# Optimization experiments

Measured on AMD Instinct MI355X. Metric: run time of the kernel, lower is better.

Reference implementation:

```python
import jax, jax.numpy as jnp
import numpy as np

N = 8192
F_IN = 690
F_OUT = 690
H = 3
ALPHA = 0.2  # LeakyReLU negative slope
NEG_INF = -9e15


def setup_inputs() -> dict:
    key = jax.random.key(0)
    k1, k2, k3, k4 = jax.random.split(key, 4)
    x = jax.random.normal(k1, (N, F_IN), dtype=jnp.float32)
    adj = jax.random.randint(k2, (N, N), 0, 2, dtype=jnp.int32)
    adj = adj.at[jnp.arange(N), jnp.arange(N)].set(1)  # self-loops, as in eye() init
    # Xavier-ish scaled params, stacked over heads
    W = jax.random.normal(k3, (H, F_IN, F_OUT), dtype=jnp.float32) * 0.05
    a = jax.random.normal(k4, (H, 2 * F_OUT, 1), dtype=jnp.float32) * 0.05
    return {"x": x, "adj": adj, "W": W, "a": a}


def reference(x, adj, W, a):
    # Wh per head: [H, N, F_OUT]
    Wh = jnp.einsum('nf,hfo->hno', x, W)
    # Additive decomposition of concat-based score: e_ij = leakyrelu(a1_i + a2_j)
    a1 = jnp.einsum('hno,ho->hn', Wh, a[:, :F_OUT, 0])  # [H, N]
    a2 = jnp.einsum('hno,ho->hn', Wh, a[:, F_OUT:, 0])  # [H, N]
    e = jax.nn.leaky_relu(a1[:, :, None] + a2[:, None, :], negative_slope=ALPHA)  # [H, N, N]
    e = jnp.where(adj[None, :, :] > 0, e, NEG_INF)
    attn = jax.nn.softmax(e, axis=-1)
    h_prime = jnp.einsum('hnm,hmo->hno', attn, Wh)  # [H, N, F_OUT]
    # GAT(concat=False): mean over heads, then ELU (dropout is identity in eval)
    y = jax.nn.elu(jnp.mean(h_prime, axis=0))  # [N, F_OUT]
    return y
```

## Files before the change

kernel.cpp:

```cpp
#include <hip/hip_runtime.h>
#include <hip/hip_bf16.h>
#include <stdint.h>

#define NN 8192
#define FD 690
#define NH 3
#define KPAD 704
#define OPAD 768
#define USTRIDE 704
#define KS 2
#define LOG2E 1.4426950408889634f

typedef __attribute__((ext_vector_type(8))) short bf16x8;
typedef __attribute__((ext_vector_type(4))) float f32x4;

typedef __attribute__((address_space(1))) const void gas_t;
typedef __attribute__((address_space(3))) void las_t;

__device__ __forceinline__ void async_ld16(const void* g, void* l) {
  __builtin_amdgcn_global_load_lds((gas_t*)g, (las_t*)l, 16, 0, 0);
}

__device__ __forceinline__ float bf2f(unsigned short u) {
  return __uint_as_float(((unsigned int)u) << 16);
}
__device__ __forceinline__ unsigned short f2bf(float f) {
  __hip_bfloat16 h = __float2bfloat16(f);
  return *reinterpret_cast<unsigned short*>(&h);
}
__device__ __forceinline__ float selbit(float e, uint32_t lo, uint32_t hi) {
  uint64_t m = ((uint64_t)hi << 32) | lo;
  float r;
  asm("v_cndmask_b32 %0, 0, %1, %2" : "=v"(r) : "v"(e), "s"(m));
  return r;
}

__global__ __launch_bounds__(256) void k_cast(const float* __restrict__ x,
                                              const float* __restrict__ W,
                                              unsigned short* __restrict__ xb,
                                              unsigned short* __restrict__ wt) {
  int idx = blockIdx.x * 256 + threadIdx.x;
  if (idx < NN * KPAD) {
    int n = idx / KPAD, f = idx - n * KPAD;
    float v = (f < FD) ? x[(size_t)n * FD + f] : 0.f;
    xb[idx] = f2bf(v);
    return;
  }
  idx -= NN * KPAD;
  if (idx >= NH * OPAD * KPAD) return;
  int h = idx / (OPAD * KPAD);
  int rem = idx - h * OPAD * KPAD;
  int o = rem / KPAD, f = rem - o * KPAD;
  float v = (o < FD && f < FD) ? W[((size_t)h * FD + f) * FD + o] : 0.f;
  wt[idx] = f2bf(v);
}

__global__ __launch_bounds__(256) void k_pack(const int* __restrict__ adj,
                                              uint64_t* __restrict__ bm) {
  int wid = (blockIdx.x * 256 + threadIdx.x) >> 6;
  int lane = threadIdx.x & 63;
  int i = wid >> 7, wj = wid & 127;
  int v = adj[(int64_t)i * NN + wj * 64 + lane];
  uint64_t m = __ballot(v > 0);
  if (lane == 0) bm[i * 128 + wj] = m;
}

__global__ __launch_bounds__(512) void k_gemm_wht(const unsigned short* __restrict__ wt,
                                                  const unsigned short* __restrict__ xb,
                                                  const float* __restrict__ a,
                                                  unsigned short* __restrict__ wht,
                                                  float* __restrict__ a1acc,
                                                  float* __restrict__ a2acc) {
  const int m0 = blockIdx.x * 128;
  const int n0 = blockIdx.y * 256;
  const int h  = blockIdx.z;
  const int tid = threadIdx.x;
  const int w = tid >> 6, l = tid & 63;
  const int wm = w >> 2, wn = w & 3;
  __shared__ unsigned short As[128 * 64];
  __shared__ unsigned short Bs[256 * 64];
  const unsigned short* Ag = wt + (size_t)h * OPAD * KPAD;
  f32x4 acc[4][4] = {};
  for (int kt = 0; kt < KPAD / 64; ++kt) {
    const int k0 = kt * 64;
#pragma unroll
    for (int r = 0; r < 2; ++r) {
      const unsigned short* g = Ag + (size_t)(m0 + r * 64 + w * 8 + (l >> 3)) * KPAD + k0 + (l & 7) * 8;
      async_ld16(g, &As[(r * 64 + w * 8) * 64]);
    }
#pragma unroll
    for (int r = 0; r < 4; ++r) {
      const unsigned short* g = xb + (size_t)(n0 + r * 64 + w * 8 + (l >> 3)) * KPAD + k0 + (l & 7) * 8;
      async_ld16(g, &Bs[(r * 64 + w * 8) * 64]);
    }
    __syncthreads();
#pragma unroll
    for (int ks = 0; ks < 2; ++ks) {
      bf16x8 af[4], bfr[4];
#pragma unroll
      for (int mi = 0; mi < 4; ++mi)
        af[mi] = *reinterpret_cast<const bf16x8*>(
            &As[(wm * 64 + mi * 16 + (l & 15)) * 64 + ks * 32 + (l >> 4) * 8]);
#pragma unroll
      for (int ni = 0; ni < 4; ++ni)
        bfr[ni] = *reinterpret_cast<const bf16x8*>(
            &Bs[(wn * 64 + ni * 16 + (l & 15)) * 64 + ks * 32 + (l >> 4) * 8]);
#pragma unroll
      for (int mi = 0; mi < 4; ++mi)
#pragma unroll
        for (int ni = 0; ni < 4; ++ni)
          acc[mi][ni] = __builtin_amdgcn_mfma_f32_16x16x32_bf16(af[mi], bfr[ni], acc[mi][ni], 0, 0, 0);
    }
    __syncthreads();
  }
  unsigned short* Wh = wht + (size_t)h * OPAD * NN;
#pragma unroll
  for (int mi = 0; mi < 4; ++mi)
#pragma unroll
    for (int j = 0; j < 4; ++j) {
      int o = m0 + wm * 64 + mi * 16 + (l >> 4) * 4 + j;
#pragma unroll
      for (int ni = 0; ni < 4; ++ni) {
        int n = n0 + wn * 64 + ni * 16 + (l & 15);
        float val = (o == FD) ? 1.0f : acc[mi][ni][j];
        Wh[(size_t)o * NN + n] = f2bf(val);
      }
    }
  const float* ap1 = a + h * 2 * FD;
  const float* ap2 = ap1 + FD;
  float av1[4][4], av2[4][4];
#pragma unroll
  for (int mi = 0; mi < 4; ++mi)
#pragma unroll
    for (int j = 0; j < 4; ++j) {
      int o = m0 + wm * 64 + mi * 16 + (l >> 4) * 4 + j;
      bool ok = (o < FD);
      av1[mi][j] = ok ? ap1[o] : 0.f;
      av2[mi][j] = ok ? ap2[o] : 0.f;
    }
#pragma unroll
  for (int ni = 0; ni < 4; ++ni) {
    float p1 = 0.f, p2 = 0.f;
#pragma unroll
    for (int mi = 0; mi < 4; ++mi)
#pragma unroll
      for (int j = 0; j < 4; ++j) {
        p1 += acc[mi][ni][j] * av1[mi][j];
        p2 += acc[mi][ni][j] * av2[mi][j];
      }
    int n = n0 + wn * 64 + ni * 16 + (l & 15);
    unsafeAtomicAdd(&a1acc[h * NN + n], p1);
    unsafeAtomicAdd(&a2acc[h * NN + n], p2);
  }
}

__global__ __launch_bounds__(256) void k_exp(const float* __restrict__ a1acc,
                                             const float* __restrict__ a2acc,
                                             float* __restrict__ e1s, float* __restrict__ f1s,
                                             float* __restrict__ e2s, float* __restrict__ f2s) {
  int i = blockIdx.x * 256 + threadIdx.x;
  if (i >= NH * NN) return;
  float s1 = a1acc[i] * LOG2E, s2 = a2acc[i] * LOG2E;
  e1s[i] = exp2f(s1);
  f1s[i] = exp2f(0.2f * s1);
  e2s[i] = exp2f(s2);
  f2s[i] = exp2f(0.2f * s2);
}

__global__ __launch_bounds__(512, 4) void k_pv(const unsigned short* __restrict__ wht,
                                               const float* __restrict__ e1s,
                                               const float* __restrict__ f1s,
                                               const float* __restrict__ e2s,
                                               const float* __restrict__ f2s,
                                               const uint64_t* __restrict__ bm,
                                               float* __restrict__ U) {
  const int m0 = blockIdx.x * 64;
  const int n0 = blockIdx.y * 384;
  const int h    = blockIdx.z / KS;
  const int kseg = blockIdx.z % KS;
  const int tid = threadIdx.x;
  const int w = tid >> 6, l = tid & 63;
  const int wu = __builtin_amdgcn_readfirstlane(w);
  __shared__ unsigned short As[64 * 64];
  __shared__ unsigned short Bs[384 * 64];
  const unsigned short* Bg = wht + (size_t)h * OPAD * NN;
  const uint64_t* bmw = bm + (size_t)(m0 + wu * 8) * 128;
  float E1v[8], F1v[8];
#pragma unroll
  for (int r = 0; r < 8; ++r) {
    E1v[r] = e1s[h * NN + m0 + wu * 8 + r];
    F1v[r] = f1s[h * NN + m0 + wu * 8 + r];
  }

  const int kt0 = kseg * (NN / 64 / KS);
  const int ktend = kt0 + NN / 64 / KS;

  f32x4 acc[4][3] = {};

  for (int kt = kt0; kt < ktend; ++kt) {
    const int k0 = kt * 64;
    const float e2v = e2s[h * NN + k0 + l];
    const float f2v = f2s[h * NN + k0 + l];
#pragma unroll
    for (int call = 0; call < 6; ++call) {
      int c = call * 512 + tid;
      int row = c >> 3;
      int kb  = c & 7;
      int kbs = kb ^ (row & 7);
      const unsigned short* g = Bg + (size_t)(n0 + row) * NN + k0 + kbs * 8;
      async_ld16(g, &Bs[(size_t)c * 8]);
    }
#pragma unroll
    for (int r = 0; r < 8; ++r) {
      uint64_t mrow = bmw[(size_t)r * 128 + kt];
      uint32_t mlo = __builtin_amdgcn_readfirstlane((uint32_t)mrow);
      uint32_t mhi = __builtin_amdgcn_readfirstlane((uint32_t)(mrow >> 32));
      float e = fmaxf(E1v[r] * e2v, F1v[r] * f2v);
      e = selbit(e, mlo, mhi);
      As[(wu * 8 + r) * 64 + (l ^ (r << 3))] = f2bf(e);
    }
    __syncthreads();

#pragma unroll
    for (int ks = 0; ks < 2; ++ks) {
      bf16x8 af[4], bfr[3];
#pragma unroll
      for (int mi = 0; mi < 4; ++mi) {
        int row = mi * 16 + (l & 15);
        af[mi] = *reinterpret_cast<const bf16x8*>(
            &As[row * 64 + (((ks * 4 + (l >> 4)) ^ (row & 7)) * 8)]);
      }
#pragma unroll
      for (int ni = 0; ni < 3; ++ni) {
        int row = w * 48 + ni * 16 + (l & 15);
        bfr[ni] = *reinterpret_cast<const bf16x8*>(
            &Bs[row * 64 + (((ks * 4 + (l >> 4)) ^ (row & 7)) * 8)]);
      }
#pragma unroll
      for (int mi = 0; mi < 4; ++mi)
#pragma unroll
        for (int ni = 0; ni < 3; ++ni)
          acc[mi][ni] = __builtin_amdgcn_mfma_f32_16x16x32_bf16(af[mi], bfr[ni], acc[mi][ni], 0, 0, 0);
    }
    __syncthreads();
  }

#pragma unroll
  for (int mi = 0; mi < 4; ++mi)
#pragma unroll
    for (int j = 0; j < 4; ++j) {
      int i = m0 + mi * 16 + (l >> 4) * 4 + j;
#pragma unroll
      for (int ni = 0; ni < 3; ++ni) {
        int n = n0 + w * 48 + ni * 16 + (l & 15);
        if (n <= FD) unsafeAtomicAdd(&U[((size_t)h * NN + i) * USTRIDE + n], acc[mi][ni][j]);
      }
    }
}

__global__ __launch_bounds__(256) void k_final(const float* __restrict__ U,
                                               float* __restrict__ y) {
  int idx = blockIdx.x * 256 + threadIdx.x;
  if (idx >= NN * (FD / 2)) return;
  int i = idx / (FD / 2), p = idx - i * (FD / 2);
  int o = p * 2;
  const size_t HS = (size_t)NN * USTRIDE;
  float s0 = 0.f, s1 = 0.f;
#pragma unroll
  for (int h = 0; h < NH; ++h) {
    size_t b = h * HS + (size_t)i * USTRIDE;
    float2 u = *reinterpret_cast<const float2*>(&U[b + o]);
    float zi = 1.0f / U[b + FD];
    s0 += u.x * zi;
    s1 += u.y * zi;
  }
  s0 *= (1.f / 3.f);
  s1 *= (1.f / 3.f);
  float2 out;
  out.x = s0 > 0.f ? s0 : (expf(s0) - 1.f);
  out.y = s1 > 0.f ? s1 : (expf(s1) - 1.f);
  *reinterpret_cast<float2*>(&y[(size_t)i * FD + o]) = out;
}

extern "C" void kernel_launch(void* const* d_in, const int* in_sizes, int n_in,
                              void* d_out, int out_size, void* d_ws, size_t ws_size,
                              hipStream_t stream) {
  const float* x   = (const float*)d_in[0];
  const int*   adj = (const int*)d_in[1];
  const float* W   = (const float*)d_in[2];
  const float* a   = (const float*)d_in[3];
  float* y = (float*)d_out;

  char* ws = (char*)d_ws;
  size_t off = 0;
  auto alloc = [&](size_t bytes) {
    void* p = ws + off;
    off = (off + bytes + 255) & ~(size_t)255;
    return p;
  };
  unsigned short* xb  = (unsigned short*)alloc((size_t)NN * KPAD * 2);
  unsigned short* wt  = (unsigned short*)alloc((size_t)NH * OPAD * KPAD * 2);
  unsigned short* wht = (unsigned short*)alloc((size_t)NH * OPAD * NN * 2);
  float* e1s = (float*)alloc((size_t)NH * NN * 4);
  float* f1s = (float*)alloc((size_t)NH * NN * 4);
  float* e2s = (float*)alloc((size_t)NH * NN * 4);
  float* f2s = (float*)alloc((size_t)NH * NN * 4);
  uint64_t* bm = (uint64_t*)alloc((size_t)NN * 128 * 8);
  float* U = (float*)alloc((size_t)NH * NN * USTRIDE * 4);
  float* a1acc = (float*)alloc((size_t)NH * NN * 4);
  float* a2acc = (float*)alloc((size_t)NH * NN * 4);
  (void)ws_size; (void)in_sizes; (void)n_in; (void)out_size;

  hipMemsetAsync(U, 0, (size_t)NH * NN * USTRIDE * 4, stream);
  hipMemsetAsync(a1acc, 0, (size_t)NH * NN * 4 * 2, stream);

  const int cast_total = NN * KPAD + NH * OPAD * KPAD;
  k_cast<<<(cast_total + 255) / 256, 256, 0, stream>>>(x, W, xb, wt);
  k_pack<<<NN * 128 / 4, 256, 0, stream>>>(adj, bm);
  k_gemm_wht<<<dim3(OPAD / 128, NN / 256, NH), 512, 0, stream>>>(wt, xb, a, wht, a1acc, a2acc);
  k_exp<<<(NH * NN + 255) / 256, 256, 0, stream>>>(a1acc, a2acc, e1s, f1s, e2s, f2s);
  k_pv<<<dim3(NN / 64, 2, NH * KS), 512, 0, stream>>>(wht, e1s, f1s, e2s, f2s, bm, U);
  k_final<<<(NN * (FD / 2) + 255) / 256, 256, 0, stream>>>(U, y);
}
```

Before: 635.7 us.

## Vectorize cast and adjacency packing, replace split-K atomics with per-split buffers

The cast kernel now converts four x elements per thread with vector loads and stores, and the adjacency packer reads int4 and builds the 64-bit masks through lane shuffles instead of one ballot per 64 ints. When the workspace is large enough, each k-split of the PV kernel writes plain stores into its own U buffer. The final kernel then sums the two buffers, which removes the large memset and the atomic adds. The cost is an extra 70 MB buffer that k_final must read back.

```diff
diff --git a/kernel.cpp b/kernel.cpp
--- a/kernel.cpp
+++ b/kernel.cpp
@@ -39,14 +39,32 @@
                                               const float* __restrict__ W,
                                               unsigned short* __restrict__ xb,
                                               unsigned short* __restrict__ wt) {
-  int idx = blockIdx.x * 256 + threadIdx.x;
-  if (idx < NN * KPAD) {
+  int q = blockIdx.x * 256 + threadIdx.x;
+  const int XQ = NN * KPAD / 4;
+  if (q < XQ) {
+    int idx = q * 4;
     int n = idx / KPAD, f = idx - n * KPAD;
-    float v = (f < FD) ? x[(size_t)n * FD + f] : 0.f;
-    xb[idx] = f2bf(v);
+    uint2 out;
+    if (f + 3 < FD) {
+      const float* xp = &x[(size_t)n * FD + f];
+      float2 a = *reinterpret_cast<const float2*>(xp);
+      float2 b = *reinterpret_cast<const float2*>(xp + 2);
+      out.x = (uint32_t)f2bf(a.x) | ((uint32_t)f2bf(a.y) << 16);
+      out.y = (uint32_t)f2bf(b.x) | ((uint32_t)f2bf(b.y) << 16);
+    } else {
+      unsigned short e[4];
+#pragma unroll
+      for (int t = 0; t < 4; ++t) {
+        int ff = f + t;
+        e[t] = (ff < FD) ? f2bf(x[(size_t)n * FD + ff]) : 0;
+      }
+      out.x = (uint32_t)e[0] | ((uint32_t)e[1] << 16);
+      out.y = (uint32_t)e[2] | ((uint32_t)e[3] << 16);
+    }
+    *reinterpret_cast<uint2*>(&xb[idx]) = out;
     return;
   }
-  idx -= NN * KPAD;
+  int idx = q - XQ;
   if (idx >= NH * OPAD * KPAD) return;
   int h = idx / (OPAD * KPAD);
   int rem = idx - h * OPAD * KPAD;
@@ -55,14 +73,20 @@
   wt[idx] = f2bf(v);
 }
 
-__global__ __launch_bounds__(256) void k_pack(const int* __restrict__ adj,
+__global__ __launch_bounds__(256) void k_pack(const int4* __restrict__ adj4,
                                               uint64_t* __restrict__ bm) {
-  int wid = (blockIdx.x * 256 + threadIdx.x) >> 6;
+  int gw = (blockIdx.x * 256 + threadIdx.x) >> 6;
   int lane = threadIdx.x & 63;
-  int i = wid >> 7, wj = wid & 127;
-  int v = adj[(int64_t)i * NN + wj * 64 + lane];
-  uint64_t m = __ballot(v > 0);
-  if (lane == 0) bm[i * 128 + wj] = m;
+  int i = gw >> 5, seg = gw & 31;
+  int4 v = adj4[(size_t)i * (NN / 4) + seg * 64 + lane];
+  uint32_t nib = (uint32_t)(v.x > 0) | ((uint32_t)(v.y > 0) << 1)
+               | ((uint32_t)(v.z > 0) << 2) | ((uint32_t)(v.w > 0) << 3);
+  nib |= __shfl_xor(nib, 1) << 4;
+  nib |= __shfl_xor(nib, 2) << 8;
+  nib |= __shfl_xor(nib, 4) << 16;
+  uint32_t hi = __shfl_xor(nib, 8);
+  if ((lane & 15) == 0)
+    bm[(size_t)i * 128 + seg * 4 + (lane >> 4)] = (uint64_t)nib | ((uint64_t)hi << 32);
 }
 
 __global__ __launch_bounds__(512) void k_gemm_wht(const unsigned short* __restrict__ wt,
@@ -173,7 +197,9 @@
                                                const float* __restrict__ e2s,
                                                const float* __restrict__ f2s,
                                                const uint64_t* __restrict__ bm,
-                                               float* __restrict__ U) {
+                                               float* __restrict__ U0,
+                                               float* __restrict__ U1,
+                                               int plain) {
   const int m0 = blockIdx.x * 64;
   const int n0 = blockIdx.y * 384;
   const int h    = blockIdx.z / KS;
@@ -245,6 +271,7 @@
     __syncthreads();
   }
 
+  float* Ud = (kseg == 0) ? U0 : U1;
 #pragma unroll
   for (int mi = 0; mi < 4; ++mi)
 #pragma unroll
@@ -253,13 +280,19 @@
 #pragma unroll
       for (int ni = 0; ni < 3; ++ni) {
         int n = n0 + w * 48 + ni * 16 + (l & 15);
-        if (n <= FD) unsafeAtomicAdd(&U[((size_t)h * NN + i) * USTRIDE + n], acc[mi][ni][j]);
-      }
-    }
-}
-
-__global__ __launch_bounds__(256) void k_final(const float* __restrict__ U,
-                                               float* __restrict__ y) {
+        if (n <= FD) {
+          size_t off = ((size_t)h * NN + i) * USTRIDE + n;
+          if (plain) Ud[off] = acc[mi][ni][j];
+          else       unsafeAtomicAdd(&U0[off], acc[mi][ni][j]);
+        }
+      }
+    }
+}
+
+__global__ __launch_bounds__(256) void k_final(const float* __restrict__ U0,
+                                               const float* __restrict__ U1,
+                                               float* __restrict__ y,
+                                               int two) {
   int idx = blockIdx.x * 256 + threadIdx.x;
   if (idx >= NN * (FD / 2)) return;
   int i = idx / (FD / 2), p = idx - i * (FD / 2);
@@ -269,8 +302,14 @@
 #pragma unroll
   for (int h = 0; h < NH; ++h) {
     size_t b = h * HS + (size_t)i * USTRIDE;
-    float2 u = *reinterpret_cast<const float2*>(&U[b + o]);
-    float zi = 1.0f / U[b + FD];
+    float2 u = *reinterpret_cast<const float2*>(&U0[b + o]);
+    float z = U0[b + FD];
+    if (two) {
+      float2 u2 = *reinterpret_cast<const float2*>(&U1[b + o]);
+      u.x += u2.x; u.y += u2.y;
+      z += U1[b + FD];
+    }
+    float zi = 1.0f / z;
     s0 += u.x * zi;
     s1 += u.y * zi;
   }
@@ -306,19 +345,23 @@
   float* e2s = (float*)alloc((size_t)NH * NN * 4);
   float* f2s = (float*)alloc((size_t)NH * NN * 4);
   uint64_t* bm = (uint64_t*)alloc((size_t)NN * 128 * 8);
-  float* U = (float*)alloc((size_t)NH * NN * USTRIDE * 4);
+  float* U0 = (float*)alloc((size_t)NH * NN * USTRIDE * 4);
   float* a1acc = (float*)alloc((size_t)NH * NN * 4);
   float* a2acc = (float*)alloc((size_t)NH * NN * 4);
-  (void)ws_size; (void)in_sizes; (void)n_in; (void)out_size;
-
-  hipMemsetAsync(U, 0, (size_t)NH * NN * USTRIDE * 4, stream);
+  const size_t usize = (size_t)NH * NN * USTRIDE * 4;
+  bool two = (ws_size >= off + usize + 256);
+  float* U1 = two ? (float*)alloc(usize) : U0;
+  (void)in_sizes; (void)n_in; (void)out_size;
+
+  if (!two) hipMemsetAsync(U0, 0, usize, stream);
   hipMemsetAsync(a1acc, 0, (size_t)NH * NN * 4 * 2, stream);
 
-  const int cast_total = NN * KPAD + NH * OPAD * KPAD;
+  const int cast_total = NN * KPAD / 4 + NH * OPAD * KPAD;
   k_cast<<<(cast_total + 255) / 256, 256, 0, stream>>>(x, W, xb, wt);
-  k_pack<<<NN * 128 / 4, 256, 0, stream>>>(adj, bm);
+  k_pack<<<NN * 32 * 64 / 256, 256, 0, stream>>>((const int4*)adj, bm);
   k_gemm_wht<<<dim3(OPAD / 128, NN / 256, NH), 512, 0, stream>>>(wt, xb, a, wht, a1acc, a2acc);
   k_exp<<<(NH * NN + 255) / 256, 256, 0, stream>>>(a1acc, a2acc, e1s, f1s, e2s, f2s);
-  k_pv<<<dim3(NN / 64, 2, NH * KS), 512, 0, stream>>>(wht, e1s, f1s, e2s, f2s, bm, U);
-  k_final<<<(NN * (FD / 2) + 255) / 256, 256, 0, stream>>>(U, y);
-}
+  k_pv<<<dim3(NN / 64, 2, NH * KS), 512, 0, stream>>>(wht, e1s, f1s, e2s, f2s, bm,
+                                                      U0, U1, two ? 1 : 0);
+  k_final<<<(NN * (FD / 2) + 255) / 256, 256, 0, stream>>>(U0, U1, y, two ? 1 : 0);
+}
```

After: 547.5 us. -13.9%, faster.
